# Kernel optimization log

Hardware: AMD Instinct MI355X
Metric: run time of the kernel (lower is better)

## Reference

```python
import jax, jax.numpy as jnp
import numpy as np

BLOCK_SIZE = 64
IN_CHANNELS = 1024
OUT_CHANNELS = 1024
O_NBLOCKS = OUT_CHANNELS // BLOCK_SIZE  # 16
I_NBLOCKS = IN_CHANNELS // BLOCK_SIZE   # 16
N_TOKENS = 32768


def setup_inputs() -> dict:
    key = jax.random.key(0)
    kx, kw = jax.random.split(key)
    x = jax.random.normal(kx, (N_TOKENS, IN_CHANNELS), dtype=jnp.float32)
    # xavier_uniform over the (o_nblocks, i_nblocks, block_size) tensor:
    # fan_in = i_nblocks * block_size, fan_out = block_size (last-dim convention)
    fan_in = I_NBLOCKS * BLOCK_SIZE
    fan_out = BLOCK_SIZE
    limit = float(np.sqrt(6.0 / (fan_in + fan_out)))
    w = jax.random.uniform(kw, (O_NBLOCKS, I_NBLOCKS, BLOCK_SIZE),
                           dtype=jnp.float32, minval=-limit, maxval=limit)
    return {"x": x, "w": w}


def _build_dense_weight(w):
    # w: (R, Q, bs). Dense W[r*bs+i, q*bs+j] = w[r, q, (i - j) mod bs]
    R, Q, bs = w.shape
    i = jnp.arange(bs)
    idx = (i[:, None] - i[None, :]) % bs          # (bs, bs) circulant index
    Wb = w[:, :, idx]                              # (R, Q, bs, bs)
    return Wb.transpose(0, 2, 1, 3).reshape(R * bs, Q * bs)  # (out, in)


def reference(x, w):
    W = _build_dense_weight(w)                     # (out_channels, in_channels)
    return x @ W.T                                 # F.linear, no bias
```

## Files before the change

kernel.cpp:

```cpp
#include <hip/hip_runtime.h>
#include <stdint.h>


#define NTOK 32768
#define NCH  1024
#define BK   64
#define NKT  (NCH / BK)

typedef short bf16x8 __attribute__((ext_vector_type(8)));
typedef float f32x4  __attribute__((ext_vector_type(4)));
typedef unsigned short u16x8 __attribute__((ext_vector_type(8)));

static __device__ __forceinline__ unsigned short f2bf(float f) {
    unsigned int u = __float_as_uint(f);
    u += 0x7FFFu + ((u >> 16) & 1u);
    return (unsigned short)(u >> 16);
}

static __device__ __forceinline__ u16x8 pack8(float4 a, float4 b) {
    u16x8 v;
    v[0]=f2bf(a.x); v[1]=f2bf(a.y); v[2]=f2bf(a.z); v[3]=f2bf(a.w);
    v[4]=f2bf(b.x); v[5]=f2bf(b.y); v[6]=f2bf(b.z); v[7]=f2bf(b.w);
    return v;
}

#define GLOAD16(gp, lp)                                                          \
    __builtin_amdgcn_global_load_lds(                                            \
        (const __attribute__((address_space(1))) unsigned int*)(gp),             \
        (__attribute__((address_space(3))) unsigned int*)(lp), 16, 0, 0)

__global__ void build_w_kernel(const float* __restrict__ w, unsigned short* __restrict__ Wb) {
    int i = blockIdx.x * blockDim.x + threadIdx.x;
    int o = i >> 7;
    int j = i & 127;
    int r = o >> 6;
    int q = j >> 3;
    const float* wrow = w + ((r * 16 + q) << 6);
    int k0 = j << 3;
    u16x8 v;
#pragma unroll
    for (int e = 0; e < 8; ++e) v[e] = f2bf(wrow[(o - (k0 + e)) & 63]);
    int js = (j & ~7) | ((j & 7) ^ (o & 7));
    *(u16x8*)(Wb + (((size_t)o) << 10) + (js << 3)) = v;
}

#define PHASE_BAR() __builtin_amdgcn_s_barrier()
#define LGKM0() asm volatile("s_waitcnt lgkmcnt(0)" ::: "memory")
#define VMCNT(n) asm volatile("s_waitcnt vmcnt(" #n ")" ::: "memory")
#define CFENCE() asm volatile("" ::: "memory")
#define SETPRIO(n) __builtin_amdgcn_s_setprio(n)
#define MFMA4(d, av, bv) d = __builtin_amdgcn_mfma_f32_16x16x32_bf16(av, bv, d, 0, 0, 0)

#define ISSUE_A(t) do {                                                          \
    const float4* _p = (const float4*)(pA + ((t) << 6));                         \
    areg[0] = _p[0]; areg[1] = _p[1]; areg[2] = _p[2]; areg[3] = _p[3];          \
    CFENCE();                                                                    \
} while (0)

#define WRITE_A(Abuf) do {                                                       \
    u16x8 _w0 = pack8(areg[0], areg[1]);                                         \
    u16x8 _w1 = pack8(areg[2], areg[3]);                                         \
    *(u16x8*)((Abuf) + aw0) = _w0;                                               \
    *(u16x8*)((Abuf) + aw1) = _w1;                                               \
    CFENCE();                                                                    \
} while (0)

#define STAGE_B(buf, t) do {                                                     \
    const char* _s = srcB + ((t) << 7);                                          \
    char* _d = (buf) + (wv << 10);                                               \
    GLOAD16(_s, _d); GLOAD16(_s + (64 << 11), _d + 8192);                        \
} while (0)

#define KCOMPUTE(Abuf, Bbuf) do {                                                \
    bf16x8 afr[4][2], bfr[2][2];                                                 \
    _Pragma("unroll") for (int m = 0; m < 4; ++m)                                \
      _Pragma("unroll") for (int ks = 0; ks < 2; ++ks)                           \
        afr[m][ks] = *(const bf16x8*)((Abuf) + a_off[ks] + m * 2048);            \
    _Pragma("unroll") for (int n = 0; n < 2; ++n)                                \
      _Pragma("unroll") for (int ks = 0; ks < 2; ++ks)                           \
        bfr[n][ks] = *(const bf16x8*)((Bbuf) + b_off[ks] + n * 2048);            \
    LGKM0();                                                                     \
    SETPRIO(1);                                                                  \
    _Pragma("unroll") for (int m = 0; m < 4; ++m)                                \
      _Pragma("unroll") for (int n = 0; n < 2; ++n) {                            \
        MFMA4(acc[m][n], afr[m][0], bfr[n][0]);                                  \
        MFMA4(acc[m][n], afr[m][1], bfr[n][1]);                                  \
      }                                                                          \
    SETPRIO(0);                                                                  \
} while (0)

__global__ void __launch_bounds__(512, 4) gemm_fused_kernel(const float* __restrict__ X,
                                                            const unsigned short* __restrict__ B,
                                                            float* __restrict__ C) {
    __shared__ __align__(16) char lds[65536];
    char* As0 = lds;
    char* As1 = lds + 16384;
    char* Bs0 = lds + 32768;
    char* Bs1 = lds + 49152;

    int tid  = threadIdx.x;
    int lane = tid & 63;
    int wv   = tid >> 6;
    int wr   = wv >> 2;
    int wc   = wv & 3;

    int cpx = gridDim.x >> 3;
    int wid = ((int)blockIdx.x & 7) * cpx + ((int)blockIdx.x >> 3);
    int tn = wid & 7, tm = wid >> 3;
    int m0 = tm * 128, n0 = tn * 128;

    const float* pA = X + ((size_t)(m0 + (tid >> 2)) << 10) + ((tid & 3) << 4);
    float4 areg[4];

    int wrow = tid >> 2;
    int j0   = (tid & 3) << 1;
    int r7   = wrow & 7;
    int aw0  = wrow * 128 + (((j0    ) ^ r7) << 4);
    int aw1  = wrow * 128 + (((j0 + 1) ^ r7) << 4);

    const char* srcB = (const char*)B + (((size_t)(n0 + (tid >> 3))) << 11) + ((tid & 7) << 4);

    int xa   = (lane & 7) << 4;
    int kq16 = (lane >> 4) << 4;
    int abase = (wr * 64 + (lane & 15)) * 128;
    int bbase = (wc * 32 + (lane & 15)) * 128;
    int a_off[2] = { abase + (kq16 ^ xa), abase + ((64 + kq16) ^ xa) };
    int b_off[2] = { bbase + (kq16 ^ xa), bbase + ((64 + kq16) ^ xa) };

    f32x4 acc[4][2] = {};

    ISSUE_A(0); STAGE_B(Bs0, 0);
    VMCNT(2);
    WRITE_A(As0);
    VMCNT(0); LGKM0();
    PHASE_BAR();

    for (int t = 0; t < NKT; t += 2) {
        ISSUE_A(t + 1); STAGE_B(Bs1, t + 1);
        KCOMPUTE(As0, Bs0);
        VMCNT(2); WRITE_A(As1);
        VMCNT(0); LGKM0(); PHASE_BAR();
        if (t + 2 < NKT) {
            ISSUE_A(t + 2); STAGE_B(Bs0, t + 2);
            KCOMPUTE(As1, Bs1);
            VMCNT(2); WRITE_A(As0);
            VMCNT(0); LGKM0(); PHASE_BAR();
        } else {
            KCOMPUTE(As1, Bs1);
        }
    }

    float* Cp = C + ((size_t)(m0 + wr * 64)) * NCH + n0 + wc * 32;
    int cc = lane & 15;
    int rr = (lane >> 4) << 2;
#pragma unroll
    for (int m = 0; m < 4; ++m)
#pragma unroll
        for (int j = 0; j < 4; ++j) {
            float* rowp = Cp + ((size_t)(m * 16 + rr + j)) * NCH;
#pragma unroll
            for (int n = 0; n < 2; ++n)
                rowp[n * 16 + cc] = acc[m][n][j];
        }
}

__global__ void naive_kernel(const float* __restrict__ x, const float* __restrict__ w,
                             float* __restrict__ out) {
    int t = blockIdx.x;
    int o = blockIdx.y * 256 + threadIdx.x;
    const float* xr = x + (size_t)t * NCH;
    int r = o >> 6, oi = o & 63;
    float s = 0.f;
    for (int q = 0; q < 16; ++q) {
        const float* wq = w + (r * 16 + q) * 64;
        const float* xq = xr + q * 64;
#pragma unroll 8
        for (int j = 0; j < 64; ++j) s += xq[j] * wq[(oi - j) & 63];
    }
    out[(size_t)t * NCH + o] = s;
}

extern "C" void kernel_launch(void* const* d_in, const int* in_sizes, int n_in,
                              void* d_out, int out_size, void* d_ws, size_t ws_size,
                              hipStream_t stream) {
    const float* x = (const float*)d_in[0];
    const float* w = (const float*)d_in[1];
    float* out = (float*)d_out;

    const size_t needW = (size_t)NCH * NCH * sizeof(unsigned short);

    if (ws_size >= needW) {
        unsigned short* Wb = (unsigned short*)d_ws;
        hipLaunchKernelGGL(build_w_kernel, dim3(NCH * 128 / 256), dim3(256), 0, stream, w, Wb);
        hipLaunchKernelGGL(gemm_fused_kernel, dim3(2048), dim3(512), 0, stream, x, Wb, out);
    } else {
        hipLaunchKernelGGL(naive_kernel, dim3(NTOK, 4), dim3(256), 0, stream, x, w, out);
    }
}
```

Measured before the change: 115.3 us.

## Load B fragments directly to registers and deepen A register prefetch pipeline

B tiles are no longer staged through LDS with global_load_lds. Each wave now loads its B MFMA fragments straight from global memory into double-buffered registers, and the weight builder drops its XOR swizzle to match. A prefetch goes two tiles ahead using two register banks, with one barrier per k-tile, and LDS use halves to 32KB. This aims to cut LDS traffic and waits, but it adds VGPR pressure and duplicated global B reads across the waves that share a column.

Result: slower. 365.9 us (+217.2%).

```diff
diff --git a/kernel.cpp b/kernel.cpp
--- a/kernel.cpp
+++ b/kernel.cpp
@@ -23,11 +23,6 @@
     v[4]=f2bf(b.x); v[5]=f2bf(b.y); v[6]=f2bf(b.z); v[7]=f2bf(b.w);
     return v;
 }
-
-#define GLOAD16(gp, lp)                                                          \
-    __builtin_amdgcn_global_load_lds(                                            \
-        (const __attribute__((address_space(1))) unsigned int*)(gp),             \
-        (__attribute__((address_space(3))) unsigned int*)(lp), 16, 0, 0)
 
 __global__ void build_w_kernel(const float* __restrict__ w, unsigned short* __restrict__ Wb) {
     int i = blockIdx.x * blockDim.x + threadIdx.x;
@@ -40,69 +35,67 @@
     u16x8 v;
 #pragma unroll
     for (int e = 0; e < 8; ++e) v[e] = f2bf(wrow[(o - (k0 + e)) & 63]);
-    int js = (j & ~7) | ((j & 7) ^ (o & 7));
-    *(u16x8*)(Wb + (((size_t)o) << 10) + (js << 3)) = v;
+    *(u16x8*)(Wb + (((size_t)o) << 10) + (j << 3)) = v;
 }
 
 #define PHASE_BAR() __builtin_amdgcn_s_barrier()
 #define LGKM0() asm volatile("s_waitcnt lgkmcnt(0)" ::: "memory")
-#define VMCNT(n) asm volatile("s_waitcnt vmcnt(" #n ")" ::: "memory")
 #define CFENCE() asm volatile("" ::: "memory")
 #define SETPRIO(n) __builtin_amdgcn_s_setprio(n)
 #define MFMA4(d, av, bv) d = __builtin_amdgcn_mfma_f32_16x16x32_bf16(av, bv, d, 0, 0, 0)
-
-#define ISSUE_A(t) do {                                                          \
+#define NOHOOK ((void)0)
+
+#define ISSUE_A(bank, t) do {                                                    \
     const float4* _p = (const float4*)(pA + ((t) << 6));                         \
-    areg[0] = _p[0]; areg[1] = _p[1]; areg[2] = _p[2]; areg[3] = _p[3];          \
-    CFENCE();                                                                    \
-} while (0)
-
-#define WRITE_A(Abuf) do {                                                       \
-    u16x8 _w0 = pack8(areg[0], areg[1]);                                         \
-    u16x8 _w1 = pack8(areg[2], areg[3]);                                         \
+    bank[0] = _p[0]; bank[1] = _p[1]; bank[2] = _p[2]; bank[3] = _p[3];          \
+} while (0)
+
+#define ISSUE_B(bank, t) do {                                                    \
+    const char* _b = pB + ((t) << 7);                                            \
+    bank[0][0] = *(const bf16x8*)(_b);                                           \
+    bank[0][1] = *(const bf16x8*)(_b + 64);                                      \
+    bank[1][0] = *(const bf16x8*)(_b + 32768);                                   \
+    bank[1][1] = *(const bf16x8*)(_b + 32768 + 64);                              \
+} while (0)
+
+#define WRITE_A(bank, Abuf) do {                                                 \
+    u16x8 _w0 = pack8(bank[0], bank[1]);                                         \
+    u16x8 _w1 = pack8(bank[2], bank[3]);                                         \
     *(u16x8*)((Abuf) + aw0) = _w0;                                               \
     *(u16x8*)((Abuf) + aw1) = _w1;                                               \
-    CFENCE();                                                                    \
-} while (0)
-
-#define STAGE_B(buf, t) do {                                                     \
-    const char* _s = srcB + ((t) << 7);                                          \
-    char* _d = (buf) + (wv << 10);                                               \
-    GLOAD16(_s, _d); GLOAD16(_s + (64 << 11), _d + 8192);                        \
-} while (0)
-
-#define KCOMPUTE(Abuf, Bbuf) do {                                                \
-    bf16x8 afr[4][2], bfr[2][2];                                                 \
+} while (0)
+
+#define FTILE(Ard, Awr, aW, IA, bC, bI, tB) do {                                 \
+    ISSUE_B(bI, tB);                                                             \
+    IA;                                                                          \
+    bf16x8 afr[4][2];                                                            \
     _Pragma("unroll") for (int m = 0; m < 4; ++m)                                \
       _Pragma("unroll") for (int ks = 0; ks < 2; ++ks)                           \
-        afr[m][ks] = *(const bf16x8*)((Abuf) + a_off[ks] + m * 2048);            \
-    _Pragma("unroll") for (int n = 0; n < 2; ++n)                                \
-      _Pragma("unroll") for (int ks = 0; ks < 2; ++ks)                           \
-        bfr[n][ks] = *(const bf16x8*)((Bbuf) + b_off[ks] + n * 2048);            \
-    LGKM0();                                                                     \
+        afr[m][ks] = *(const bf16x8*)((Ard) + a_off[ks] + m * 2048);             \
+    WRITE_A(aW, Awr);                                                            \
     SETPRIO(1);                                                                  \
     _Pragma("unroll") for (int m = 0; m < 4; ++m)                                \
       _Pragma("unroll") for (int n = 0; n < 2; ++n) {                            \
-        MFMA4(acc[m][n], afr[m][0], bfr[n][0]);                                  \
-        MFMA4(acc[m][n], afr[m][1], bfr[n][1]);                                  \
+        MFMA4(acc[m][n], afr[m][0], bC[n][0]);                                   \
+        MFMA4(acc[m][n], afr[m][1], bC[n][1]);                                   \
       }                                                                          \
     SETPRIO(0);                                                                  \
+    LGKM0(); PHASE_BAR(); CFENCE();                                              \
 } while (0)
 
 __global__ void __launch_bounds__(512, 4) gemm_fused_kernel(const float* __restrict__ X,
                                                             const unsigned short* __restrict__ B,
                                                             float* __restrict__ C) {
-    __shared__ __align__(16) char lds[65536];
+    __shared__ __align__(16) char lds[32768];
     char* As0 = lds;
     char* As1 = lds + 16384;
-    char* Bs0 = lds + 32768;
-    char* Bs1 = lds + 49152;
 
     int tid  = threadIdx.x;
     int lane = tid & 63;
     int wv   = tid >> 6;
     int wr   = wv >> 2;
     int wc   = wv & 3;
+    (void)wv;
 
     int cpx = gridDim.x >> 3;
     int wid = ((int)blockIdx.x & 7) * cpx + ((int)blockIdx.x >> 3);
@@ -110,7 +103,11 @@
     int m0 = tm * 128, n0 = tn * 128;
 
     const float* pA = X + ((size_t)(m0 + (tid >> 2)) << 10) + ((tid & 3) << 4);
-    float4 areg[4];
+    float4 aregE[4], aregO[4];
+
+    const char* pB = (const char*)B + (((size_t)(n0 + wc * 32 + (lane & 15))) << 11)
+                     + ((lane >> 4) << 4);
+    bf16x8 bBE[2][2], bBO[2][2];
 
     int wrow = tid >> 2;
     int j0   = (tid & 3) << 1;
@@ -118,36 +115,40 @@
     int aw0  = wrow * 128 + (((j0    ) ^ r7) << 4);
     int aw1  = wrow * 128 + (((j0 + 1) ^ r7) << 4);
 
-    const char* srcB = (const char*)B + (((size_t)(n0 + (tid >> 3))) << 11) + ((tid & 7) << 4);
-
     int xa   = (lane & 7) << 4;
     int kq16 = (lane >> 4) << 4;
     int abase = (wr * 64 + (lane & 15)) * 128;
-    int bbase = (wc * 32 + (lane & 15)) * 128;
     int a_off[2] = { abase + (kq16 ^ xa), abase + ((64 + kq16) ^ xa) };
-    int b_off[2] = { bbase + (kq16 ^ xa), bbase + ((64 + kq16) ^ xa) };
 
     f32x4 acc[4][2] = {};
 
-    ISSUE_A(0); STAGE_B(Bs0, 0);
-    VMCNT(2);
-    WRITE_A(As0);
-    VMCNT(0); LGKM0();
-    PHASE_BAR();
-
-    for (int t = 0; t < NKT; t += 2) {
-        ISSUE_A(t + 1); STAGE_B(Bs1, t + 1);
-        KCOMPUTE(As0, Bs0);
-        VMCNT(2); WRITE_A(As1);
-        VMCNT(0); LGKM0(); PHASE_BAR();
-        if (t + 2 < NKT) {
-            ISSUE_A(t + 2); STAGE_B(Bs0, t + 2);
-            KCOMPUTE(As1, Bs1);
-            VMCNT(2); WRITE_A(As0);
-            VMCNT(0); LGKM0(); PHASE_BAR();
-        } else {
-            KCOMPUTE(As1, Bs1);
-        }
+    ISSUE_B(bBE, 0);
+    ISSUE_A(aregE, 0);
+    ISSUE_A(aregO, 1);
+    WRITE_A(aregE, As0);
+    LGKM0(); PHASE_BAR(); CFENCE();
+
+    for (int t = 0; t < NKT - 2; t += 2) {
+        FTILE(As0, As1, aregO, ISSUE_A(aregE, t + 2), bBE, bBO, t + 1);
+        FTILE(As1, As0, aregE, ISSUE_A(aregO, t + 3), bBO, bBE, t + 2);
+    }
+    FTILE(As0, As1, aregO, NOHOOK, bBE, bBO, NKT - 1);
+    {
+        bf16x8 afr[4][2];
+#pragma unroll
+        for (int m = 0; m < 4; ++m)
+#pragma unroll
+            for (int ks = 0; ks < 2; ++ks)
+                afr[m][ks] = *(const bf16x8*)(As1 + a_off[ks] + m * 2048);
+        SETPRIO(1);
+#pragma unroll
+        for (int m = 0; m < 4; ++m)
+#pragma unroll
+            for (int n = 0; n < 2; ++n) {
+                MFMA4(acc[m][n], afr[m][0], bBO[n][0]);
+                MFMA4(acc[m][n], afr[m][1], bBO[n][1]);
+            }
+        SETPRIO(0);
     }
 
     float* Cp = C + ((size_t)(m0 + wr * 64)) * NCH + n0 + wc * 32;
```
